# Kernel optimization log

Hardware: AMD Instinct MI355X
Metric: run time of the kernel (lower is better)

Reference implementation:

```python
import jax, jax.numpy as jnp
import numpy as np

CUTOFF = 5.2
BUCKETS_PER_CUTOFF = 1
BOX = 100.0
N_ATOMS = 100000
EXTRA_SPACE = 1e-5

# half-shell neighbor displacements: cartesian_prod(arange(-b,1)^3)[:-1] -> 7 vectors for b=1
_d1 = np.arange(-BUCKETS_PER_CUTOFF, 1)
DISPLACEMENTS = jnp.asarray(
    np.stack(np.meshgrid(_d1, _d1, _d1, indexing='ij'), axis=-1).reshape(-1, 3)[:-1],
    dtype=jnp.int32)  # (7, 3)
NUM_NEIGHBORS = DISPLACEMENTS.shape[0]


def setup_inputs() -> dict:
    key = jax.random.key(0)
    k1, _ = jax.random.split(key)
    # uniform in [0, 0.999*BOX) so fractional coordinates are strictly < 1
    coordinates = jax.random.uniform(k1, (1, N_ATOMS, 3), dtype=jnp.float32) * (BOX * 0.999)
    cell = jnp.eye(3, dtype=jnp.float32) * BOX
    return {"coordinates": coordinates, "cell": cell}


def _cumsum_from_zero(x):
    return jnp.concatenate([jnp.zeros((1,), x.dtype), jnp.cumsum(x[:-1])])


def reference(coordinates, cell):
    n_atoms = coordinates.shape[1]
    cell_diag = jnp.diagonal(cell)                       # (3,)
    bucket_length = CUTOFF / BUCKETS_PER_CUTOFF + EXTRA_SPACE
    grid = jnp.floor(cell_diag / bucket_length).astype(jnp.int32) + 1   # shape_buckets_grid (3,)
    total_buckets = int(grid[0] * grid[1] * grid[2])
    # faithful to source: [g1*g2, g1, 1]
    scaling = jnp.array([grid[1] * grid[2], grid[1], 1], dtype=jnp.int32)

    # fractionalize + main bucket vector/flat indices
    frac = coordinates / cell_diag.reshape(1, 1, -1)     # (1, N, 3)
    vec_idx = jnp.round(frac * (grid - 1).astype(frac.dtype)).astype(jnp.int32)  # (1, N, 3)
    flat = (vec_idx * scaling).sum(-1).reshape(-1)       # (N,) main_bucket_flat_index

    # image-index converters (stable argsort by bucket)
    imidx_from_atidx = jnp.argsort(flat)                 # jax argsort is stable
    atidx_from_imidx = jnp.argsort(imidx_from_atidx)

    # per-bucket counts / exclusive cumcounts
    counts = jnp.bincount(flat, length=total_buckets)
    cumcounts = _cumsum_from_zero(counts)
    max_in_bucket = int(counts.max())

    # ---- within-image pairs ----
    wp_idx = jnp.nonzero(counts > 1)[0]
    wp_count = counts[wp_idx]
    wp_cum = cumcounts[wp_idx]
    pu, pl = jnp.triu_indices(max_in_bucket, k=1)
    pairs = jnp.stack([pu, pl]).astype(jnp.int32)        # (2, P)
    # sort_along_row(row_for_sorting=1): key = upper + lower*max_in_bucket
    order = jnp.argsort(pairs[0] + pairs[1] * max_in_bucket)
    pairs = pairs[:, order]
    padded = pairs[None] + wp_cum.reshape(-1, 1, 1)      # (B, 2, P)
    padded = jnp.transpose(padded, (1, 0, 2)).reshape(2, -1)
    max_pairs = max_in_bucket * (max_in_bucket - 1) // 2
    mask = (jnp.arange(max_pairs)[None, :] < (wp_count * (wp_count - 1) // 2)[:, None]).reshape(-1)
    within_image_pairs = jnp.stack([padded[0][mask], padded[1][mask]])  # (2, n_pairs)

    # ---- between-image 'lower' indices ----
    neigh_vec = vec_idx[:, :, None, :] + DISPLACEMENTS   # (1, N, 7, 3)
    neigh_vec = jnp.mod(neigh_vec, grid)                 # pbc wrap of neighbor buckets
    neigh_flat = (neigh_vec * scaling).sum(-1)           # (1, N, 7)
    n_count = counts[neigh_flat]                         # (1, N, 7)
    n_cum = cumcounts[neigh_flat]                        # (1, N, 7)
    pad = jnp.broadcast_to(
        jnp.arange(max_in_bucket, dtype=n_cum.dtype).reshape(1, 1, 1, -1),
        (1, n_atoms, NUM_NEIGHBORS, max_in_bucket))      # (1, N, 7, M) -- dominant intermediate
    m = pad < n_count[..., None]
    lower_between = (pad + n_cum[..., None])[m]          # (n_between,)

    return within_image_pairs, lower_between, frac, imidx_from_atidx, atidx_from_imidx
```

## Files before the change

kernel.cpp:

```cpp
#include <hip/hip_runtime.h>
#include <hip/hip_bf16.h>

#define NB_MAX 8192
#define NTHR 256

__device__ __forceinline__ void get_grid(const float* __restrict__ cell,
                                         int& g0, int& g1, int& g2,
                                         float& d0, float& d1, float& d2) {
  d0 = cell[0]; d1 = cell[4]; d2 = cell[8];
  const float bl = (float)(5.2 + 1e-05);
  g0 = (int)floorf(d0 / bl) + 1;
  g1 = (int)floorf(d1 / bl) + 1;
  g2 = (int)floorf(d2 / bl) + 1;
}

__device__ __forceinline__ void atom_vec(const float* __restrict__ coord, int a,
                                         float d0, float d1, float d2,
                                         int g0, int g1, int g2,
                                         int& v0, int& v1, int& v2) {
  float x = coord[3 * a + 0], y = coord[3 * a + 1], z = coord[3 * a + 2];
  float fx = x / d0, fy = y / d1, fz = z / d2;
  v0 = (int)rintf(fx * (float)(g0 - 1));
  v1 = (int)rintf(fy * (float)(g1 - 1));
  v2 = (int)rintf(fz * (float)(g2 - 1));
}

__global__ void k_bucket_count(const float* __restrict__ coord,
                               const float* __restrict__ cell,
                               float* __restrict__ out_frac,
                               int* __restrict__ flat,
                               int* __restrict__ counts, int n) {
  int a = blockIdx.x * blockDim.x + threadIdx.x;
  if (a >= n) return;
  int g0, g1, g2; float d0, d1, d2;
  get_grid(cell, g0, g1, g2, d0, d1, d2);
  float x = coord[3 * a + 0], y = coord[3 * a + 1], z = coord[3 * a + 2];
  float fx = x / d0, fy = y / d1, fz = z / d2;
  out_frac[3 * a + 0] = fx;
  out_frac[3 * a + 1] = fy;
  out_frac[3 * a + 2] = fz;
  int v0 = (int)rintf(fx * (float)(g0 - 1));
  int v1 = (int)rintf(fy * (float)(g1 - 1));
  int v2 = (int)rintf(fz * (float)(g2 - 1));
  int b = v0 * (g1 * g2) + v1 * g1 + v2;
  flat[a] = b;
  atomicAdd(&counts[b], 1);
}

__global__ __launch_bounds__(1024) void k_scan_buckets(
    const float* __restrict__ cell,
    const int* __restrict__ counts,
    int* __restrict__ cumc,
    int* __restrict__ pairoff,
    int* __restrict__ scalars) {
  int g0, g1, g2; float d0, d1, d2;
  get_grid(cell, g0, g1, g2, d0, d1, d2);
  int nb = g0 * g1 * g2;
  const int T = 1024, IT = NB_MAX / 1024;
  __shared__ int sc[T], sp[T];
  int t = threadIdx.x;
  int base = t * IT;
  int cv[IT];
  int lc = 0, lp = 0;
  for (int i = 0; i < IT; ++i) {
    int idx = base + i;
    int c = (idx < nb) ? counts[idx] : 0;
    cv[i] = c;
    lc += c;
    lp += c * (c - 1) / 2;
  }
  sc[t] = lc; sp[t] = lp;
  __syncthreads();
  for (int off = 1; off < T; off <<= 1) {
    int vc = 0, vp = 0;
    if (t >= off) { vc = sc[t - off]; vp = sp[t - off]; }
    __syncthreads();
    sc[t] += vc; sp[t] += vp;
    __syncthreads();
  }
  int ec = sc[t] - lc, ep = sp[t] - lp;
  for (int i = 0; i < IT; ++i) {
    int idx = base + i;
    if (idx < nb) { cumc[idx] = ec; pairoff[idx] = ep; }
    ec += cv[i];
    ep += cv[i] * (cv[i] - 1) / 2;
  }
  if (t == T - 1) scalars[0] = sp[T - 1];
}

__global__ void k_scatter(const int* __restrict__ flat,
                          const int* __restrict__ cumc,
                          int* __restrict__ fill,
                          int* __restrict__ sorted, int n) {
  int a = blockIdx.x * blockDim.x + threadIdx.x;
  if (a >= n) return;
  int b = flat[a];
  int pos = cumc[b] + atomicAdd(&fill[b], 1);
  sorted[pos] = a;
}

__global__ void k_sort_buckets(const float* __restrict__ cell,
                               const int* __restrict__ counts,
                               const int* __restrict__ cumc,
                               int* __restrict__ sorted) {
  int lane = threadIdx.x & 63;
  int b = blockIdx.x * 4 + (threadIdx.x >> 6);
  int g0, g1, g2; float d0, d1, d2;
  get_grid(cell, g0, g1, g2, d0, d1, d2);
  int nb = g0 * g1 * g2;
  if (b >= nb) return;
  int c = counts[b];
  if (c < 2) return;
  int s = cumc[b];
  if (c <= 64) {
    int val = (lane < c) ? sorted[s + lane] : 0x7fffffff;
    int rank = 0;
    for (int j = 0; j < c; ++j) {
      int other = __shfl(val, j);
      rank += (other < val) ? 1 : 0;
    }
    if (lane < c) sorted[s + rank] = val;
  } else if (lane == 0) {
    for (int i = 1; i < c; ++i) {
      int key = sorted[s + i];
      int j = i - 1;
      while (j >= 0 && sorted[s + j] > key) {
        sorted[s + j + 1] = sorted[s + j];
        --j;
      }
      sorted[s + j + 1] = key;
    }
  }
}

__global__ void k_pairs(const float* __restrict__ cell,
                        const int* __restrict__ counts,
                        const int* __restrict__ cumc,
                        const int* __restrict__ pairoff,
                        const int* __restrict__ scalars,
                        float* __restrict__ out) {
  int lane = threadIdx.x & 63;
  int b = blockIdx.x * 4 + (threadIdx.x >> 6);
  int g0, g1, g2; float d0, d1, d2;
  get_grid(cell, g0, g1, g2, d0, d1, d2);
  int nb = g0 * g1 * g2;
  if (b >= nb) return;
  int c = counts[b];
  if (c < 2) return;
  int cum = cumc[b];
  int off = pairoff[b];
  int P = scalars[0];
  int np = c * (c - 1) / 2;
  for (int k = lane; k < np; k += 64) {
    int l = (int)((1.0f + sqrtf(1.0f + 8.0f * (float)k)) * 0.5f);
    while (l * (l - 1) / 2 > k) --l;
    while ((l + 1) * l / 2 <= k) ++l;
    int u = k - l * (l - 1) / 2;
    out[off + k] = (float)(cum + u);
    out[P + off + k] = (float)(cum + l);
  }
}

__global__ void k_perm(const int* __restrict__ sorted,
                       float* __restrict__ out_im,
                       float* __restrict__ out_at, int n) {
  int i = blockIdx.x * blockDim.x + threadIdx.x;
  if (i >= n) return;
  int a = sorted[i];
  out_im[i] = (float)a;
  out_at[a] = (float)i;
}

__global__ void k_runlen(const float* __restrict__ coord,
                         const float* __restrict__ cell,
                         const int* __restrict__ counts,
                         int* __restrict__ Sarr,
                         int* __restrict__ blockpart, int n) {
  __shared__ int sm[NTHR];
  int t = threadIdx.x;
  int a = blockIdx.x * NTHR + t;
  int S = 0;
  if (a < n) {
    int g0, g1, g2; float d0, d1, d2;
    get_grid(cell, g0, g1, g2, d0, d1, d2);
    int v0, v1, v2;
    atom_vec(coord, a, d0, d1, d2, g0, g1, g2, v0, v1, v2);
    for (int m = 0; m < 7; ++m) {
      int dx = ((m >> 2) & 1) ? 0 : -1;
      int dy = ((m >> 1) & 1) ? 0 : -1;
      int dz = (m & 1) ? 0 : -1;
      int nx = v0 + dx; if (nx < 0) nx += g0;
      int ny = v1 + dy; if (ny < 0) ny += g1;
      int nz = v2 + dz; if (nz < 0) nz += g2;
      int nb_ = nx * (g1 * g2) + ny * g1 + nz;
      S += counts[nb_];
    }
    Sarr[a] = S;
  }
  sm[t] = S;
  __syncthreads();
  for (int off = NTHR / 2; off > 0; off >>= 1) {
    if (t < off) sm[t] += sm[t + off];
    __syncthreads();
  }
  if (t == 0) blockpart[blockIdx.x] = sm[0];
}

__global__ __launch_bounds__(1024) void k_scan_partials(
    const int* __restrict__ blockpart,
    int* __restrict__ blockoff,
    int* __restrict__ scalars, int nblocks) {
  const int T = 1024;
  __shared__ int sm[T];
  int t = threadIdx.x;
  int v = (t < nblocks) ? blockpart[t] : 0;
  sm[t] = v;
  __syncthreads();
  for (int off = 1; off < T; off <<= 1) {
    int x = 0;
    if (t >= off) x = sm[t - off];
    __syncthreads();
    sm[t] += x;
    __syncthreads();
  }
  blockoff[t] = sm[t] - v;
  if (t == T - 1) scalars[1] = sm[T - 1];
}

__global__ void k_emit(const float* __restrict__ coord,
                       const float* __restrict__ cell,
                       const int* __restrict__ counts,
                       const int* __restrict__ cumc,
                       const int* __restrict__ Sarr,
                       const int* __restrict__ blockoff,
                       const int* __restrict__ scalars,
                       float* __restrict__ out, int n) {
  __shared__ int sm[NTHR];
  int t = threadIdx.x;
  int a = blockIdx.x * NTHR + t;
  int S = (a < n) ? Sarr[a] : 0;
  sm[t] = S;
  __syncthreads();
  for (int off = 1; off < NTHR; off <<= 1) {
    int x = 0;
    if (t >= off) x = sm[t - off];
    __syncthreads();
    sm[t] += x;
    __syncthreads();
  }
  int excl = sm[t] - S;
  if (a >= n) return;
  int g0, g1, g2; float d0, d1, d2;
  get_grid(cell, g0, g1, g2, d0, d1, d2);
  int v0, v1, v2;
  atom_vec(coord, a, d0, d1, d2, g0, g1, g2, v0, v1, v2);
  long base = 2L * (long)scalars[0] + (long)blockoff[blockIdx.x] + (long)excl;
  int k = 0;
  for (int m = 0; m < 7; ++m) {
    int dx = ((m >> 2) & 1) ? 0 : -1;
    int dy = ((m >> 1) & 1) ? 0 : -1;
    int dz = (m & 1) ? 0 : -1;
    int nx = v0 + dx; if (nx < 0) nx += g0;
    int ny = v1 + dy; if (ny < 0) ny += g1;
    int nz = v2 + dz; if (nz < 0) nz += g2;
    int nb_ = nx * (g1 * g2) + ny * g1 + nz;
    int c = counts[nb_];
    int cum = cumc[nb_];
    for (int j = 0; j < c; ++j) {
      out[base + k] = (float)(cum + j);
      ++k;
    }
  }
}

extern "C" void kernel_launch(void* const* d_in, const int* in_sizes, int n_in,
                              void* d_out, int out_size, void* d_ws, size_t ws_size,
                              hipStream_t stream) {
  const float* coord = (const float*)d_in[0];
  const float* cell = (const float*)d_in[1];
  float* out = (float*)d_out;
  int n = in_sizes[0] / 3;

  int* W = (int*)d_ws;
  int* counts = W;
  int* fill = W + NB_MAX;
  int* scalars = W + 2 * NB_MAX;
  int* cumc = W + 2 * NB_MAX + 16;
  int* pairoff = cumc + NB_MAX;
  int* flat = pairoff + NB_MAX;
  int* sorted = flat + n;
  int* Sarr = sorted + n;
  int* blockpart = Sarr + n;
  int* blockoff = blockpart + 1024;

  float* out_frac = out + (out_size - 5 * n);
  float* out_im = out + (out_size - 2 * n);
  float* out_at = out + (out_size - n);

  int nblocks = (n + NTHR - 1) / NTHR;

  hipMemsetAsync(d_ws, 0, (size_t)(2 * NB_MAX + 16) * sizeof(int), stream);

  k_bucket_count<<<nblocks, NTHR, 0, stream>>>(coord, cell, out_frac, flat, counts, n);
  k_scan_buckets<<<1, 1024, 0, stream>>>(cell, counts, cumc, pairoff, scalars);
  k_scatter<<<nblocks, NTHR, 0, stream>>>(flat, cumc, fill, sorted, n);
  k_sort_buckets<<<NB_MAX / 4, 256, 0, stream>>>(cell, counts, cumc, sorted);
  k_pairs<<<NB_MAX / 4, 256, 0, stream>>>(cell, counts, cumc, pairoff, scalars, out);
  k_perm<<<nblocks, NTHR, 0, stream>>>(sorted, out_im, out_at, n);
  k_runlen<<<nblocks, NTHR, 0, stream>>>(coord, cell, counts, Sarr, blockpart, n);
  k_scan_partials<<<1, 1024, 0, stream>>>(blockpart, blockoff, scalars, nblocks);
  k_emit<<<nblocks, NTHR, 0, stream>>>(coord, cell, counts, cumc, Sarr, blockoff, scalars, out, n);
}
```

Baseline: 141.2 us.

## Fuse sort/perm/pairs kernels, use wave-shuffle scans, emit neighbors one wavefront per atom

Replaces the shared-memory Hillis-Steele scans with wavefront shuffle scans in the bucket and partial scans. Merges bucket sorting, the permutation outputs and within-bucket pair generation into one kernel. Splits the emit step into an offsets kernel and a wave-per-atom emit, so each atom's roughly 90 neighbor indices are written by 64 lanes in a coalesced way instead of a serial per-thread loop. This adds one kernel launch and extra index arithmetic per output element, and many lanes sit idle when an atom's segment is short.

```diff
diff --git a/kernel.cpp b/kernel.cpp
--- a/kernel.cpp
+++ b/kernel.cpp
@@ -57,8 +57,9 @@
   get_grid(cell, g0, g1, g2, d0, d1, d2);
   int nb = g0 * g1 * g2;
   const int T = 1024, IT = NB_MAX / 1024;
-  __shared__ int sc[T], sp[T];
+  __shared__ int wc[16], wp[16];
   int t = threadIdx.x;
+  int lane = t & 63, wid = t >> 6;
   int base = t * IT;
   int cv[IT];
   int lc = 0, lp = 0;
@@ -69,23 +70,35 @@
     lc += c;
     lp += c * (c - 1) / 2;
   }
-  sc[t] = lc; sp[t] = lp;
-  __syncthreads();
-  for (int off = 1; off < T; off <<= 1) {
-    int vc = 0, vp = 0;
-    if (t >= off) { vc = sc[t - off]; vp = sp[t - off]; }
-    __syncthreads();
-    sc[t] += vc; sp[t] += vp;
-    __syncthreads();
-  }
-  int ec = sc[t] - lc, ep = sp[t] - lp;
+  int ic = lc, ip = lp;
+  for (int off = 1; off < 64; off <<= 1) {
+    int yc = __shfl_up(ic, off);
+    int yp = __shfl_up(ip, off);
+    if (lane >= off) { ic += yc; ip += yp; }
+  }
+  if (lane == 63) { wc[wid] = ic; wp[wid] = ip; }
+  __syncthreads();
+  if (wid == 0 && lane < 16) {
+    int vc2 = wc[lane], vp2 = wp[lane];
+    int sc2 = vc2, sp2 = vp2;
+    for (int off = 1; off < 16; off <<= 1) {
+      int yc = __shfl_up(sc2, off);
+      int yp = __shfl_up(sp2, off);
+      if (lane >= off) { sc2 += yc; sp2 += yp; }
+    }
+    wc[lane] = sc2 - vc2;
+    wp[lane] = sp2 - vp2;
+  }
+  __syncthreads();
+  int ec = wc[wid] + (ic - lc);
+  int ep = wp[wid] + (ip - lp);
   for (int i = 0; i < IT; ++i) {
     int idx = base + i;
     if (idx < nb) { cumc[idx] = ec; pairoff[idx] = ep; }
     ec += cv[i];
     ep += cv[i] * (cv[i] - 1) / 2;
   }
-  if (t == T - 1) scalars[0] = sp[T - 1];
+  if (t == T - 1) scalars[0] = ep;
 }
 
 __global__ void k_scatter(const int* __restrict__ flat,
@@ -99,10 +112,15 @@
   sorted[pos] = a;
 }
 
-__global__ void k_sort_buckets(const float* __restrict__ cell,
-                               const int* __restrict__ counts,
-                               const int* __restrict__ cumc,
-                               int* __restrict__ sorted) {
+__global__ void k_sort_perm_pairs(const float* __restrict__ cell,
+                                  const int* __restrict__ counts,
+                                  const int* __restrict__ cumc,
+                                  const int* __restrict__ pairoff,
+                                  const int* __restrict__ scalars,
+                                  int* __restrict__ sorted,
+                                  float* __restrict__ out_im,
+                                  float* __restrict__ out_at,
+                                  float* __restrict__ out) {
   int lane = threadIdx.x & 63;
   int b = blockIdx.x * 4 + (threadIdx.x >> 6);
   int g0, g1, g2; float d0, d1, d2;
@@ -110,8 +128,16 @@
   int nb = g0 * g1 * g2;
   if (b >= nb) return;
   int c = counts[b];
-  if (c < 2) return;
+  if (c == 0) return;
   int s = cumc[b];
+  if (c == 1) {
+    if (lane == 0) {
+      int a = sorted[s];
+      out_im[s] = (float)a;
+      out_at[a] = (float)s;
+    }
+    return;
+  }
   if (c <= 64) {
     int val = (lane < c) ? sorted[s + lane] : 0x7fffffff;
     int rank = 0;
@@ -119,7 +145,11 @@
       int other = __shfl(val, j);
       rank += (other < val) ? 1 : 0;
     }
-    if (lane < c) sorted[s + rank] = val;
+    if (lane < c) {
+      sorted[s + rank] = val;
+      out_im[s + rank] = (float)val;
+      out_at[val] = (float)(s + rank);
+    }
   } else if (lane == 0) {
     for (int i = 1; i < c; ++i) {
       int key = sorted[s + i];
@@ -130,24 +160,12 @@
       }
       sorted[s + j + 1] = key;
     }
-  }
-}
-
-__global__ void k_pairs(const float* __restrict__ cell,
-                        const int* __restrict__ counts,
-                        const int* __restrict__ cumc,
-                        const int* __restrict__ pairoff,
-                        const int* __restrict__ scalars,
-                        float* __restrict__ out) {
-  int lane = threadIdx.x & 63;
-  int b = blockIdx.x * 4 + (threadIdx.x >> 6);
-  int g0, g1, g2; float d0, d1, d2;
-  get_grid(cell, g0, g1, g2, d0, d1, d2);
-  int nb = g0 * g1 * g2;
-  if (b >= nb) return;
-  int c = counts[b];
-  if (c < 2) return;
-  int cum = cumc[b];
+    for (int i = 0; i < c; ++i) {
+      int a = sorted[s + i];
+      out_im[s + i] = (float)a;
+      out_at[a] = (float)(s + i);
+    }
+  }
   int off = pairoff[b];
   int P = scalars[0];
   int np = c * (c - 1) / 2;
@@ -156,19 +174,9 @@
     while (l * (l - 1) / 2 > k) --l;
     while ((l + 1) * l / 2 <= k) ++l;
     int u = k - l * (l - 1) / 2;
-    out[off + k] = (float)(cum + u);
-    out[P + off + k] = (float)(cum + l);
-  }
-}
-
-__global__ void k_perm(const int* __restrict__ sorted,
-                       float* __restrict__ out_im,
-                       float* __restrict__ out_at, int n) {
-  int i = blockIdx.x * blockDim.x + threadIdx.x;
-  if (i >= n) return;
-  int a = sorted[i];
-  out_im[i] = (float)a;
-  out_at[a] = (float)i;
+    out[off + k] = (float)(s + u);
+    out[P + off + k] = (float)(s + l);
+  }
 }
 
 __global__ void k_runlen(const float* __restrict__ coord,
@@ -210,52 +218,76 @@
     const int* __restrict__ blockpart,
     int* __restrict__ blockoff,
     int* __restrict__ scalars, int nblocks) {
-  const int T = 1024;
-  __shared__ int sm[T];
+  __shared__ int ws[16];
   int t = threadIdx.x;
+  int lane = t & 63, wid = t >> 6;
   int v = (t < nblocks) ? blockpart[t] : 0;
-  sm[t] = v;
-  __syncthreads();
-  for (int off = 1; off < T; off <<= 1) {
-    int x = 0;
-    if (t >= off) x = sm[t - off];
-    __syncthreads();
-    sm[t] += x;
-    __syncthreads();
-  }
-  blockoff[t] = sm[t] - v;
-  if (t == T - 1) scalars[1] = sm[T - 1];
-}
-
-__global__ void k_emit(const float* __restrict__ coord,
-                       const float* __restrict__ cell,
-                       const int* __restrict__ counts,
-                       const int* __restrict__ cumc,
-                       const int* __restrict__ Sarr,
-                       const int* __restrict__ blockoff,
-                       const int* __restrict__ scalars,
-                       float* __restrict__ out, int n) {
-  __shared__ int sm[NTHR];
+  int iv = v;
+  for (int off = 1; off < 64; off <<= 1) {
+    int y = __shfl_up(iv, off);
+    if (lane >= off) iv += y;
+  }
+  if (lane == 63) ws[wid] = iv;
+  __syncthreads();
+  if (wid == 0 && lane < 16) {
+    int v2 = ws[lane], s2 = v2;
+    for (int off = 1; off < 16; off <<= 1) {
+      int y = __shfl_up(s2, off);
+      if (lane >= off) s2 += y;
+    }
+    ws[lane] = s2 - v2;
+  }
+  __syncthreads();
+  int excl = ws[wid] + (iv - v);
+  blockoff[t] = excl;
+  if (t == 1023) scalars[1] = excl + v;
+}
+
+__global__ void k_offsets(const int* __restrict__ Sarr,
+                          const int* __restrict__ blockoff,
+                          int* __restrict__ Oarr, int n) {
+  __shared__ int ws[4];
   int t = threadIdx.x;
+  int lane = t & 63, wid = t >> 6;
   int a = blockIdx.x * NTHR + t;
   int S = (a < n) ? Sarr[a] : 0;
-  sm[t] = S;
-  __syncthreads();
-  for (int off = 1; off < NTHR; off <<= 1) {
-    int x = 0;
-    if (t >= off) x = sm[t - off];
-    __syncthreads();
-    sm[t] += x;
-    __syncthreads();
-  }
-  int excl = sm[t] - S;
+  int iv = S;
+  for (int off = 1; off < 64; off <<= 1) {
+    int y = __shfl_up(iv, off);
+    if (lane >= off) iv += y;
+  }
+  if (lane == 63) ws[wid] = iv;
+  __syncthreads();
+  if (wid == 0 && lane < 4) {
+    int v2 = ws[lane], s2 = v2;
+    for (int off = 1; off < 4; off <<= 1) {
+      int y = __shfl_up(s2, off);
+      if (lane >= off) s2 += y;
+    }
+    ws[lane] = s2 - v2;
+  }
+  __syncthreads();
+  if (a < n) Oarr[a] = blockoff[blockIdx.x] + ws[wid] + (iv - S);
+}
+
+__global__ void k_emit_wave(const float* __restrict__ coord,
+                            const float* __restrict__ cell,
+                            const int* __restrict__ counts,
+                            const int* __restrict__ cumc,
+                            const int* __restrict__ Oarr,
+                            const int* __restrict__ scalars,
+                            float* __restrict__ out, int n) {
+  int a = (blockIdx.x * blockDim.x + threadIdx.x) >> 6;
+  int lane = threadIdx.x & 63;
   if (a >= n) return;
   int g0, g1, g2; float d0, d1, d2;
   get_grid(cell, g0, g1, g2, d0, d1, d2);
   int v0, v1, v2;
   atom_vec(coord, a, d0, d1, d2, g0, g1, g2, v0, v1, v2);
-  long base = 2L * (long)scalars[0] + (long)blockoff[blockIdx.x] + (long)excl;
-  int k = 0;
+  int segs[8];
+  int cums[7];
+  segs[0] = 0;
+#pragma unroll
   for (int m = 0; m < 7; ++m) {
     int dx = ((m >> 2) & 1) ? 0 : -1;
     int dy = ((m >> 1) & 1) ? 0 : -1;
@@ -264,12 +296,18 @@
     int ny = v1 + dy; if (ny < 0) ny += g1;
     int nz = v2 + dz; if (nz < 0) nz += g2;
     int nb_ = nx * (g1 * g2) + ny * g1 + nz;
-    int c = counts[nb_];
-    int cum = cumc[nb_];
-    for (int j = 0; j < c; ++j) {
-      out[base + k] = (float)(cum + j);
-      ++k;
-    }
+    cums[m] = cumc[nb_];
+    segs[m + 1] = segs[m] + counts[nb_];
+  }
+  int S = segs[7];
+  long base = 2L * (long)scalars[0] + (long)Oarr[a];
+  for (int p = lane; p < S; p += 64) {
+    int v = cums[0] + p;
+#pragma unroll
+    for (int m = 1; m < 7; ++m) {
+      if (p >= segs[m]) v = cums[m] + (p - segs[m]);
+    }
+    out[base + p] = (float)v;
   }
 }
 
@@ -292,6 +330,7 @@
   int* Sarr = sorted + n;
   int* blockpart = Sarr + n;
   int* blockoff = blockpart + 1024;
+  int* Oarr = blockoff + 1024;
 
   float* out_frac = out + (out_size - 5 * n);
   float* out_im = out + (out_size - 2 * n);
@@ -304,10 +343,10 @@
   k_bucket_count<<<nblocks, NTHR, 0, stream>>>(coord, cell, out_frac, flat, counts, n);
   k_scan_buckets<<<1, 1024, 0, stream>>>(cell, counts, cumc, pairoff, scalars);
   k_scatter<<<nblocks, NTHR, 0, stream>>>(flat, cumc, fill, sorted, n);
-  k_sort_buckets<<<NB_MAX / 4, 256, 0, stream>>>(cell, counts, cumc, sorted);
-  k_pairs<<<NB_MAX / 4, 256, 0, stream>>>(cell, counts, cumc, pairoff, scalars, out);
-  k_perm<<<nblocks, NTHR, 0, stream>>>(sorted, out_im, out_at, n);
+  k_sort_perm_pairs<<<NB_MAX / 4, 256, 0, stream>>>(cell, counts, cumc, pairoff, scalars,
+                                                    sorted, out_im, out_at, out);
   k_runlen<<<nblocks, NTHR, 0, stream>>>(coord, cell, counts, Sarr, blockpart, n);
   k_scan_partials<<<1, 1024, 0, stream>>>(blockpart, blockoff, scalars, nblocks);
-  k_emit<<<nblocks, NTHR, 0, stream>>>(coord, cell, counts, cumc, Sarr, blockoff, scalars, out, n);
-}
+  k_offsets<<<nblocks, NTHR, 0, stream>>>(Sarr, blockoff, Oarr, n);
+  k_emit_wave<<<(n + 3) / 4, 256, 0, stream>>>(coord, cell, counts, cumc, Oarr, scalars, out, n);
+}
```

Result: slower. 148.3 us (+5.0%).
